# Kernel tuning notes

Hardware: AMD Instinct MI355X
Metric: run time of the kernel (lower is better)

## Reference

```python
import jax, jax.numpy as jnp
import numpy as np

ANNEALING_SCALE = 0.1
BS, NV, S, D, V = 2, 16, 1024, 768, 50257

def setup_inputs() -> dict:
    key = jax.random.key(0)
    k1, k2, k3, k4, k5 = jax.random.split(key, 5)
    return {
        "input_ids": jax.random.randint(k1, (BS, S), 0, V),
        "content": jax.random.normal(k2, (BS, NV, S, D), dtype=jnp.float32),
        "contextualization": jax.random.normal(k3, (BS, NV, S, S), dtype=jnp.float32) * 0.05,
        "lm_head_weight": jax.random.normal(k4, (V, D), dtype=jnp.float32) * 0.02,
        "content_weights": jax.random.uniform(k5, (V, NV), dtype=jnp.float32),
    }

def reference(input_ids, content, contextualization, lm_head_weight, content_weights):
    bs, nv, s, d = content.shape
    # --- mask_annealing ---
    # Original computes relu(content @ W.T) over full vocab then gathers at input_ids.
    # Equivalent: gather rows of W first, then contract (same math since relu is
    # elementwise and only gathered columns are summed).
    Wg = lm_head_weight[input_ids]                              # (bs, s, d)
    sims = jnp.einsum('bkid,bjd->bkij', content, Wg)            # (bs, 16, s, s)
    sims = jnp.sum(jax.nn.relu(sims), axis=3)                   # (bs, 16, s)
    scores = jax.nn.sigmoid(-ANNEALING_SCALE * sims + 6.0)
    # upweight_nearby modifier
    scores = scores * (1.0 + jnp.arange(s, dtype=content.dtype) / 100.0)[None, None, :]
    scores = jnp.transpose(scores, (0, 2, 1))                   # (bs, s, 16)
    # --- create_content_soft_mask ---
    cw = content_weights[input_ids]                             # (bs, s, 16)
    weights = cw * scores + (1.0 - scores)                      # (bs, s, 16)
    # --- weighted sense combination ---
    content_m = content * jnp.transpose(weights, (0, 2, 1))[..., None]  # (bs,16,s,d)
    hidden = jnp.einsum('bkij,bkjd->bid', contextualization, content_m) # (bs, s, d)
    logits = hidden @ lm_head_weight.T                          # (bs, s, vocab)
    return logits
```

## Files before the change

kernel.cpp:

```cpp
#include <hip/hip_runtime.h>
#include <cstdint>
#include <cstddef>

#define BSZ 2
#define NV 16
#define SEQ 1024
#define DIM 768
#define VOC 50257
#define VOCP 50304

typedef unsigned int u32;
typedef unsigned short u16;
typedef _Float16 half8 __attribute__((ext_vector_type(8)));
typedef float f32x4 __attribute__((ext_vector_type(4)));

__device__ __forceinline__ u16 f2h(float f) {
  return __builtin_bit_cast(unsigned short, (_Float16)f);
}
__device__ __forceinline__ u32 pk2h(float a, float b) {
  return (u32)f2h(a) | ((u32)f2h(b) << 16);
}

__global__ void k_prep_content(const float* __restrict__ content,
                               u16* __restrict__ cbf, u16* __restrict__ cT) {
  __shared__ u16 tile[32][33];
  const int bk = blockIdx.z;
  const int d0 = blockIdx.x * 32, j0 = blockIdx.y * 32;
  const float* src = content + (size_t)bk * SEQ * DIM;
  u16* dst = cbf + (size_t)bk * SEQ * DIM;
  u16* dstT = cT + (size_t)bk * DIM * SEQ;
  const int c = threadIdx.x;
#pragma unroll
  for (int rr = 0; rr < 4; ++rr) {
    const int r = threadIdx.y * 4 + rr;
    const float v = src[(size_t)(j0 + r) * DIM + d0 + c];
    const u16 bv = f2h(v);
    dst[(size_t)(j0 + r) * DIM + d0 + c] = bv;
    tile[r][c] = bv;
  }
  __syncthreads();
#pragma unroll
  for (int rr = 0; rr < 4; ++rr) {
    const int r = threadIdx.y * 4 + rr;
    dstT[(size_t)(d0 + r) * SEQ + j0 + c] = tile[c][r];
  }
}

__global__ void k_prep_w(const float* __restrict__ W, u16* __restrict__ Wb) {
  const int v = blockIdx.x;
  const int c = threadIdx.x * 4;
  u32 lo, hi;
  if (v < VOC) {
    const float4 f = *(const float4*)(W + (size_t)v * DIM + c);
    lo = pk2h(f.x, f.y); hi = pk2h(f.z, f.w);
  } else {
    lo = 0u; hi = 0u;
  }
  *(uint2*)(Wb + (size_t)v * DIM + c) = make_uint2(lo, hi);
}

__global__ void k_gather(const int* __restrict__ ids, const u16* __restrict__ Wb,
                         u16* __restrict__ Wg) {
  const int b = blockIdx.y, j = blockIdx.x;
  const int row = ids[b * SEQ + j];
  const int c = threadIdx.x * 4;
  *(uint2*)(Wg + ((size_t)b * SEQ + j) * DIM + c) =
      *(const uint2*)(Wb + (size_t)row * DIM + c);
}

__global__ void k_zero(float* __restrict__ p, int n) {
  const int i = blockIdx.x * 256 + threadIdx.x;
  if (i < n) p[i] = 0.f;
}

template <int LDA, int LDB>
__device__ __forceinline__ void gemm_ktile(const u16* __restrict__ A,
                                           const u16* __restrict__ B, int ksteps,
                                           u16* As, u16* Bs, f32x4 (&acc)[4][4],
                                           int t) {
  const int lane = t & 63, w = t >> 6, wr = w >> 1, wc = w & 1;
  const int row2 = t >> 1, half = (t & 1) * 16;
  const int kl = (lane >> 4) * 8, rl = lane & 15;
  for (int kt = 0; kt < ksteps; ++kt) {
    const uint4* pa = (const uint4*)(A + (size_t)row2 * LDA + kt * 32 + half);
    const uint4* pb = (const uint4*)(B + (size_t)row2 * LDB + kt * 32 + half);
    const uint4 a0 = pa[0], a1 = pa[1];
    const uint4 b0 = pb[0], b1 = pb[1];
    __syncthreads();
    uint4* qa = (uint4*)(As + row2 * 32 + half);
    qa[0] = a0; qa[1] = a1;
    uint4* qb = (uint4*)(Bs + row2 * 32 + half);
    qb[0] = b0; qb[1] = b1;
    __syncthreads();
    half8 af[4], bf[4];
#pragma unroll
    for (int m = 0; m < 4; ++m)
      af[m] = *(const half8*)(As + (wr * 64 + m * 16 + rl) * 32 + kl);
#pragma unroll
    for (int n = 0; n < 4; ++n)
      bf[n] = *(const half8*)(Bs + (wc * 64 + n * 16 + rl) * 32 + kl);
#pragma unroll
    for (int m = 0; m < 4; ++m)
#pragma unroll
      for (int n = 0; n < 4; ++n)
        acc[m][n] = __builtin_amdgcn_mfma_f32_16x16x32_f16(af[m], bf[n], acc[m][n], 0, 0, 0);
  }
}

__global__ __launch_bounds__(256) void k_sims(const u16* __restrict__ cbf,
                                              const u16* __restrict__ Wg,
                                              float* __restrict__ sims) {
  __shared__ __align__(16) u16 As[128 * 32];
  __shared__ __align__(16) u16 Bs[128 * 32];
  const int bk = blockIdx.z, b = bk >> 4;
  const int t = threadIdx.x;
  const u16* A = cbf + (size_t)bk * SEQ * DIM + (size_t)(blockIdx.y * 128) * DIM;
  const u16* B = Wg + (size_t)b * SEQ * DIM + (size_t)(blockIdx.x * 128) * DIM;
  f32x4 acc[4][4] = {};
  gemm_ktile<DIM, DIM>(A, B, DIM / 32, As, Bs, acc, t);
  const int lane = t & 63, w = t >> 6, wr = w >> 1;
  const int rg = lane >> 4, cl = lane & 15;
#pragma unroll
  for (int m = 0; m < 4; ++m) {
#pragma unroll
    for (int r = 0; r < 4; ++r) {
      float s = 0.f;
#pragma unroll
      for (int n = 0; n < 4; ++n) {
        const float v = acc[m][n][r];
        s += fmaxf(v, 0.f);
      }
      s += __shfl_xor(s, 1);
      s += __shfl_xor(s, 2);
      s += __shfl_xor(s, 4);
      s += __shfl_xor(s, 8);
      if (cl == 0) {
        const int i = blockIdx.y * 128 + wr * 64 + m * 16 + rg * 4 + r;
        atomicAdd(&sims[(size_t)bk * SEQ + i], s);
      }
    }
  }
}

__global__ void k_weights(const float* __restrict__ sims, const int* __restrict__ ids,
                          const float* __restrict__ cw, float* __restrict__ wtsT) {
  const int j = blockIdx.x * 256 + threadIdx.x;
  const int bk = blockIdx.y;
  const int b = bk >> 4, k = bk & 15;
  const float sm = sims[(size_t)bk * SEQ + j];
  float score = 1.f / (1.f + __expf(0.1f * sm - 6.f));
  score *= 1.f + (float)j * 0.01f;
  const int id = ids[b * SEQ + j];
  const float c = cw[(size_t)id * NV + k];
  wtsT[(size_t)bk * SEQ + j] = c * score + (1.f - score);
}

__global__ void k_ctx(const float* __restrict__ ctx, const float* __restrict__ wtsT,
                      u16* __restrict__ ctxw) {
  const size_t i = ((size_t)blockIdx.x * 256 + threadIdx.x) * 4;
  const float4 c = *(const float4*)(ctx + i);
  const size_t bk = i >> 20;
  const int j = (int)(i & (SEQ - 1));
  const float4 wv = *(const float4*)(wtsT + bk * SEQ + j);
  *(uint2*)(ctxw + i) =
      make_uint2(pk2h(c.x * wv.x, c.y * wv.y), pk2h(c.z * wv.z, c.w * wv.w));
}

__global__ __launch_bounds__(256) void k_hidden(const u16* __restrict__ ctxw,
                                                const u16* __restrict__ cT,
                                                float* __restrict__ part) {
  __shared__ __align__(16) u16 As[128 * 32];
  __shared__ __align__(16) u16 Bs[128 * 32];
  const int z = blockIdx.z;
  const int b = z >> 3, ks = z & 7;
  const int i0 = blockIdx.y * 128, d0 = blockIdx.x * 128;
  const int t = threadIdx.x;
  f32x4 acc[4][4] = {};
  for (int kk = 0; kk < 2; ++kk) {
    const int sense = ks * 2 + kk;
    const u16* A = ctxw + ((size_t)(b * NV + sense) * SEQ + i0) * SEQ;
    const u16* B = cT + ((size_t)(b * NV + sense) * DIM + d0) * SEQ;
    gemm_ktile<SEQ, SEQ>(A, B, SEQ / 32, As, Bs, acc, t);
  }
  const int lane = t & 63, w = t >> 6, wr = w >> 1, wc = w & 1;
  const int rg = lane >> 4, cl = lane & 15;
  float* P = part + ((size_t)(ks * BSZ + b) * SEQ + i0) * DIM + d0;
#pragma unroll
  for (int m = 0; m < 4; ++m)
#pragma unroll
    for (int n = 0; n < 4; ++n)
#pragma unroll
      for (int r = 0; r < 4; ++r)
        P[(size_t)(wr * 64 + m * 16 + rg * 4 + r) * DIM + wc * 64 + n * 16 + cl] =
            acc[m][n][r];
}

__global__ void k_reduce(const float* __restrict__ part, u16* __restrict__ hid) {
  const size_t i = ((size_t)blockIdx.x * 256 + threadIdx.x) * 4;
  const size_t NHID = (size_t)BSZ * SEQ * DIM;
  float4 s = {0.f, 0.f, 0.f, 0.f};
#pragma unroll
  for (int g = 0; g < 8; ++g) {
    const float4 p = *(const float4*)(part + (size_t)g * NHID + i);
    s.x += p.x; s.y += p.y; s.z += p.z; s.w += p.w;
  }
  *(uint2*)(hid + i) = make_uint2(pk2h(s.x, s.y), pk2h(s.z, s.w));
}

__global__ __launch_bounds__(256) void k_logits(const u16* __restrict__ hid,
                                                const u16* __restrict__ Wb,
                                                float* __restrict__ out) {
  __shared__ __align__(16) u16 As[128 * 32];
  __shared__ __align__(16) u16 Bs[128 * 32];
  const int i0 = blockIdx.x * 128, v0 = blockIdx.y * 128;
  const int t = threadIdx.x;
  const u16* A = hid + (size_t)i0 * DIM;
  const u16* B = Wb + (size_t)v0 * DIM;
  f32x4 acc[4][4] = {};
  gemm_ktile<DIM, DIM>(A, B, DIM / 32, As, Bs, acc, t);
  const int lane = t & 63, w = t >> 6, wr = w >> 1, wc = w & 1;
  const int rg = lane >> 4, cl = lane & 15;
#pragma unroll
  for (int m = 0; m < 4; ++m)
#pragma unroll
    for (int n = 0; n < 4; ++n) {
      const int vv = v0 + wc * 64 + n * 16 + cl;
      if (vv < VOC) {
#pragma unroll
        for (int r = 0; r < 4; ++r) {
          const int i = i0 + wr * 64 + m * 16 + rg * 4 + r;
          out[(size_t)i * VOC + vv] = acc[m][n][r];
        }
      }
    }
}

extern "C" void kernel_launch(void* const* d_in, const int* in_sizes, int n_in,
                              void* d_out, int out_size, void* d_ws, size_t ws_size,
                              hipStream_t stream) {
  const int* ids = (const int*)d_in[0];
  const float* content = (const float*)d_in[1];
  const float* ctx = (const float*)d_in[2];
  const float* W = (const float*)d_in[3];
  const float* cw = (const float*)d_in[4];
  float* out = (float*)d_out;
  char* ws = (char*)d_ws;

  u16* cbf  = (u16*)(ws);
  u16* cT   = (u16*)(ws + 50331648);
  u16* Wb   = (u16*)(ws + 100663296);
  u16* Wg   = (u16*)(ws + 177930240);
  u16* ctxw = (u16*)(ws + 181075968);
  float* sims = (float*)(ws + 248184832);
  float* wtsT = (float*)(ws + 248315904);
  float* part = (float*)cbf;
  u16* hid = Wg;

  k_prep_content<<<dim3(DIM / 32, SEQ / 32, BSZ * NV), dim3(32, 8), 0, stream>>>(
      content, cbf, cT);
  k_prep_w<<<VOCP, 192, 0, stream>>>(W, Wb);
  k_gather<<<dim3(SEQ, BSZ), 192, 0, stream>>>(ids, Wb, Wg);
  k_zero<<<128, 256, 0, stream>>>(sims, BSZ * NV * SEQ);
  k_sims<<<dim3(8, 8, BSZ * NV), 256, 0, stream>>>(cbf, Wg, sims);
  k_weights<<<dim3(4, BSZ * NV), 256, 0, stream>>>(sims, ids, cw, wtsT);
  k_ctx<<<32768, 256, 0, stream>>>(ctx, wtsT, ctxw);
  k_hidden<<<dim3(6, 8, 16), 256, 0, stream>>>(ctxw, cT, part);
  k_reduce<<<1536, 256, 0, stream>>>(part, hid);
  k_logits<<<dim3(16, 393), 256, 0, stream>>>(hid, Wb, out);
}
```

Baseline: 648.5 us.

## Load GEMM tiles directly into LDS and halve hidden split-K partitions

Replaces the register-staged global-to-shared tile copies in the shared GEMM k-loop with direct global_load_lds 16-byte transfers, so data no longer passes through VGPRs. Separately, k_hidden now gives each block four senses instead of two, which halves the number of partial-sum buffers written and read by k_reduce. The first change cuts register pressure and instruction count in all three GEMMs. The second leaves k_hidden with 384 blocks, which may underfill the GPU, and the LDS layout must match the lane ordering that global_load_lds uses.

```diff
diff --git a/kernel.cpp b/kernel.cpp
--- a/kernel.cpp
+++ b/kernel.cpp
@@ -19,6 +19,12 @@
 }
 __device__ __forceinline__ u32 pk2h(float a, float b) {
   return (u32)f2h(a) | ((u32)f2h(b) << 16);
+}
+
+__device__ __forceinline__ void gload16(const u16* g, u16* l) {
+  __builtin_amdgcn_global_load_lds(
+      (const __attribute__((address_space(1))) void*)g,
+      (__attribute__((address_space(3))) void*)l, 16, 0, 0);
 }
 
 __global__ void k_prep_content(const float* __restrict__ content,
@@ -79,18 +85,20 @@
                                            u16* As, u16* Bs, f32x4 (&acc)[4][4],
                                            int t) {
   const int lane = t & 63, w = t >> 6, wr = w >> 1, wc = w & 1;
-  const int row2 = t >> 1, half = (t & 1) * 16;
   const int kl = (lane >> 4) * 8, rl = lane & 15;
+  const int srow = t >> 2;
+  const int scol = (t & 3) * 8;
+  u16* lA = As + w * 512;
+  u16* lB = Bs + w * 512;
+  const u16* ga = A + (size_t)srow * LDA + scol;
+  const u16* gb = B + (size_t)srow * LDB + scol;
   for (int kt = 0; kt < ksteps; ++kt) {
-    const uint4* pa = (const uint4*)(A + (size_t)row2 * LDA + kt * 32 + half);
-    const uint4* pb = (const uint4*)(B + (size_t)row2 * LDB + kt * 32 + half);
-    const uint4 a0 = pa[0], a1 = pa[1];
-    const uint4 b0 = pb[0], b1 = pb[1];
     __syncthreads();
-    uint4* qa = (uint4*)(As + row2 * 32 + half);
-    qa[0] = a0; qa[1] = a1;
-    uint4* qb = (uint4*)(Bs + row2 * 32 + half);
-    qb[0] = b0; qb[1] = b1;
+    gload16(ga, lA);
+    gload16(ga + (size_t)64 * LDA, lA + 2048);
+    gload16(gb, lB);
+    gload16(gb + (size_t)64 * LDB, lB + 2048);
+    ga += 32; gb += 32;
     __syncthreads();
     half8 af[4], bf[4];
 #pragma unroll
@@ -172,19 +180,19 @@
   __shared__ __align__(16) u16 As[128 * 32];
   __shared__ __align__(16) u16 Bs[128 * 32];
   const int z = blockIdx.z;
-  const int b = z >> 3, ks = z & 7;
+  const int b = z >> 2, g = z & 3;
   const int i0 = blockIdx.y * 128, d0 = blockIdx.x * 128;
   const int t = threadIdx.x;
   f32x4 acc[4][4] = {};
-  for (int kk = 0; kk < 2; ++kk) {
-    const int sense = ks * 2 + kk;
+  for (int kk = 0; kk < 4; ++kk) {
+    const int sense = g * 4 + kk;
     const u16* A = ctxw + ((size_t)(b * NV + sense) * SEQ + i0) * SEQ;
     const u16* B = cT + ((size_t)(b * NV + sense) * DIM + d0) * SEQ;
     gemm_ktile<SEQ, SEQ>(A, B, SEQ / 32, As, Bs, acc, t);
   }
   const int lane = t & 63, w = t >> 6, wr = w >> 1, wc = w & 1;
   const int rg = lane >> 4, cl = lane & 15;
-  float* P = part + ((size_t)(ks * BSZ + b) * SEQ + i0) * DIM + d0;
+  float* P = part + ((size_t)(g * BSZ + b) * SEQ + i0) * DIM + d0;
 #pragma unroll
   for (int m = 0; m < 4; ++m)
 #pragma unroll
@@ -200,7 +208,7 @@
   const size_t NHID = (size_t)BSZ * SEQ * DIM;
   float4 s = {0.f, 0.f, 0.f, 0.f};
 #pragma unroll
-  for (int g = 0; g < 8; ++g) {
+  for (int g = 0; g < 4; ++g) {
     const float4 p = *(const float4*)(part + (size_t)g * NHID + i);
     s.x += p.x; s.y += p.y; s.z += p.z; s.w += p.w;
   }
@@ -264,7 +272,7 @@
   k_sims<<<dim3(8, 8, BSZ * NV), 256, 0, stream>>>(cbf, Wg, sims);
   k_weights<<<dim3(4, BSZ * NV), 256, 0, stream>>>(sims, ids, cw, wtsT);
   k_ctx<<<32768, 256, 0, stream>>>(ctx, wtsT, ctxw);
-  k_hidden<<<dim3(6, 8, 16), 256, 0, stream>>>(ctxw, cT, part);
+  k_hidden<<<dim3(6, 8, 8), 256, 0, stream>>>(ctxw, cT, part);
   k_reduce<<<1536, 256, 0, stream>>>(part, hid);
   k_logits<<<dim3(16, 393), 256, 0, stream>>>(hid, Wb, out);
 }
```

Measured after the change: 669.1 us. +3.2%, slower.
